# Performance work log

Hardware: AMD Instinct MI355X
Metric: run time of the kernel (lower is better)

## Reference

```python
import jax, jax.numpy as jnp
import numpy as np

NUM_HEADS = 16
HEAD_DIM = 64  # d_model // num_heads = 1024 // 16
NUM_BUCKETS = 20


def setup_inputs() -> dict:
    key = jax.random.key(0)
    ks = jax.random.split(key, 5)
    B, S, D = 2, 2048, 1024
    v = jax.random.normal(ks[0], (B, S, D), dtype=jnp.float32)
    k = jax.random.normal(ks[1], (B, S, D), dtype=jnp.float32)
    q = jax.random.normal(ks[2], (B, S, D), dtype=jnp.float32)
    mask = jax.random.randint(ks[3], (B, S, S), 0, 2).astype(jnp.bool_)
    diff_matrix = jax.random.randint(ks[4], (B, S, S), 0, NUM_BUCKETS)
    rel_bias = jax.random.normal(jax.random.fold_in(key, 7), (NUM_BUCKETS, NUM_HEADS), dtype=jnp.float32)
    return {"v": v, "k": k, "q": q, "mask": mask, "diff_matrix": diff_matrix, "rel_bias": rel_bias}


def _split_heads(x):
    B, S, _ = x.shape
    return x.reshape(B, S, NUM_HEADS, HEAD_DIM).transpose(0, 2, 1, 3)  # [B,H,S,hd]


def reference(v, k, q, mask, diff_matrix, rel_bias):
    B, S, D = q.shape
    qh, kh, vh = _split_heads(q), _split_heads(k), _split_heads(v)
    scale = 1.0 / jnp.sqrt(jnp.float32(HEAD_DIM))
    scores = jnp.einsum('bhqd,bhkd->bhqk', qh, kh) * scale  # [B,H,S,S]
    # relative bias: gather [B,S,S,H] -> [B,H,S,S]
    bias = rel_bias[diff_matrix].transpose(0, 3, 1, 2)
    att = jax.nn.silu(scores + bias)
    att = jnp.where(mask[:, None, :, :], att, 0.0)
    av = jnp.einsum('bhqk,bhkd->bhqd', att, vh)  # [B,H,S,hd]
    return av.transpose(0, 2, 1, 3).reshape(B, S, D)
```

## Files before the change

kernel.cpp:

```cpp
#include <hip/hip_runtime.h>
#include <hip/hip_fp16.h>
#include <cstdint>
#include <cstddef>

#define SEQ 2048
#define DM 1024
#define NH 16
#define NB 20

typedef _Float16 half8 __attribute__((ext_vector_type(8)));
typedef _Float16 half4 __attribute__((ext_vector_type(4)));
typedef _Float16 h2v __attribute__((ext_vector_type(2)));
typedef float f32x4 __attribute__((ext_vector_type(4)));
typedef int i32x4 __attribute__((ext_vector_type(4)));
typedef unsigned int u32;
typedef unsigned int u32x2 __attribute__((ext_vector_type(2)));

#define KF_HALVES 4194304
#define VF_HALVES 4194304

__global__ __launch_bounds__(256) void pa_prep(
    const float* __restrict__ v, const float* __restrict__ k,
    const int* __restrict__ diff, const int* __restrict__ mask,
    _Float16* __restrict__ KF, _Float16* __restrict__ VF,
    unsigned char* __restrict__ PB) {
  const int bid = blockIdx.x, tid = threadIdx.x;
  if (bid < 2048) {
    int img = bid >> 4;
    int bb = img >> 6, kt = img & 63;
    int tix = ((bid & 15) << 8) | tid;
    int r = tix >> 7;
    int c0 = (tix & 127) << 3;
    const float* src = k + ((size_t)(bb * SEQ + kt * 32 + r)) * DM + c0;
    f32x4 a = *(const f32x4*)src;
    f32x4 c = *(const f32x4*)(src + 4);
    half8 o = {(_Float16)a[0], (_Float16)a[1], (_Float16)a[2], (_Float16)a[3],
               (_Float16)c[0], (_Float16)c[1], (_Float16)c[2], (_Float16)c[3]};
    int h = c0 >> 6, dh = (c0 >> 5) & 1, g4 = (c0 >> 3) & 3;
    int k2 = r >> 4, l16 = r & 15;
    int lane = g4 * 16 + l16;
    size_t off = ((size_t)((bb * 16 + h) * 64 + kt)) * 2048 + (k2 * 2 + dh) * 512 + lane * 8;
    *(half8*)(KF + off) = o;
  } else if (bid < 3072) {
    int b3 = bid - 2048;
    int img = b3 >> 3;
    int bb = img >> 6, kt = img & 63;
    int tix = ((b3 & 7) << 8) | tid;
    int kq = tix >> 8;
    int k2 = kq >> 2, g4 = kq & 3;
    int d0 = (tix & 255) << 2;
    const float* src = v + ((size_t)(bb * SEQ + kt * 32 + k2 * 16 + g4 * 4)) * DM + d0;
    f32x4 m0 = *(const f32x4*)(src);
    f32x4 m1 = *(const f32x4*)(src + DM);
    f32x4 m2 = *(const f32x4*)(src + 2 * DM);
    f32x4 m3 = *(const f32x4*)(src + 3 * DM);
#pragma unroll
    for (int i = 0; i < 4; ++i) {
      int d = d0 + i;
      int l16 = d & 15, dt = (d >> 4) & 3, dtp = dt >> 1, w = dt & 1, h = d >> 6;
      int lane = g4 * 16 + l16;
      half4 o = {(_Float16)m0[i], (_Float16)m1[i], (_Float16)m2[i], (_Float16)m3[i]};
      size_t off = ((size_t)((bb * 16 + h) * 64 + kt)) * 2048 + (k2 * 2 + dtp) * 512 + lane * 8 + w * 4;
      *(half4*)(VF + off) = o;
    }
  } else {
    int b4 = bid - 3072;
    int job = b4 >> 5;
    int bb = job >> 6, qblk = job & 63;
    int tix = ((b4 & 31) << 8) | tid;
    int kt = tix >> 7;
    int rem = tix & 127;
    int g4 = rem & 3, l16 = (rem >> 2) & 15, qs = rem >> 6;
    int lane = g4 * 16 + l16;
    int qrow = qblk * 32 + qs * 16 + l16;
    size_t rowbase = ((size_t)(bb * SEQ + qrow)) * SEQ;
    u32x2 wds;
#pragma unroll
    for (int k2 = 0; k2 < 2; ++k2) {
      int kk = kt * 32 + k2 * 16 + g4 * 4;
      i32x4 dv = *(const i32x4*)(diff + rowbase + kk);
      i32x4 mv = *(const i32x4*)(mask + rowbase + kk);
      u32 wd = 0;
#pragma unroll
      for (int r = 0; r < 4; ++r) {
        u32 byte = mv[r] ? ((u32)dv[r] << 2) : 80u;
        wd |= byte << (8 * r);
      }
      wds[k2] = wd;
    }
    size_t off = ((size_t)job) * 65536 + (size_t)kt * 1024 + (size_t)lane * 16 + (size_t)qs * 8;
    *(u32x2*)(PB + off) = wds;
  }
}

__device__ __forceinline__ half4 silu4(const f32x4& s, u32 u, int rbi) {
  float b0 = __int_as_float(__builtin_amdgcn_ds_bpermute((int)(u & 0xffu), rbi));
  float b1 = __int_as_float(__builtin_amdgcn_ds_bpermute((int)((u >> 8) & 0xffu), rbi));
  float b2 = __int_as_float(__builtin_amdgcn_ds_bpermute((int)((u >> 16) & 0xffu), rbi));
  float b3 = __int_as_float(__builtin_amdgcn_ds_bpermute((int)(u >> 24), rbi));
  h2v x01 = __builtin_bit_cast(h2v, __builtin_amdgcn_cvt_pkrtz(s[0], s[1])) +
            __builtin_bit_cast(h2v, __builtin_amdgcn_cvt_pkrtz(b0, b1));
  h2v x23 = __builtin_bit_cast(h2v, __builtin_amdgcn_cvt_pkrtz(s[2], s[3])) +
            __builtin_bit_cast(h2v, __builtin_amdgcn_cvt_pkrtz(b2, b3));
  const h2v NL2E = {(_Float16)-1.44269504f, (_Float16)-1.44269504f};
  const h2v ONE = {(_Float16)1.0f, (_Float16)1.0f};
  h2v m01 = x01 * NL2E, m23 = x23 * NL2E;
  h2v e01 = __builtin_bit_cast(h2v, h2exp2(__builtin_bit_cast(__half2, m01)));
  h2v e23 = __builtin_bit_cast(h2v, h2exp2(__builtin_bit_cast(__half2, m23)));
  h2v d01 = e01 + ONE, d23 = e23 + ONE;
  h2v y01 = x01 * __builtin_bit_cast(h2v, h2rcp(__builtin_bit_cast(__half2, d01)));
  h2v y23 = x23 * __builtin_bit_cast(h2v, h2rcp(__builtin_bit_cast(__half2, d23)));
  return (half4){y01[0], y01[1], y23[0], y23[1]};
}

__global__ __launch_bounds__(256, 4) void pa_main(
    const _Float16* __restrict__ KF, const _Float16* __restrict__ VF,
    const unsigned char* __restrict__ PB, const float* __restrict__ q,
    const float* __restrict__ relbias, float* __restrict__ out) {
  const int tid = threadIdx.x, lane = tid & 63, wid = tid >> 6;
  const int l16 = lane & 15, g4 = lane >> 4;
  const int L = (blockIdx.x & 7) * 128 + (blockIdx.x >> 3);
  const int h = L & 15;
  const int qgrp = (L >> 4) & 15;
  const int ksp = (L >> 8) & 1;
  const int b = L >> 9;
  const int qblk = qgrp * 4 + wid;
  const int qbase = qblk * 32;

  const float rbv = (lane < NB) ? relbias[lane * NH + h] : -30000.0f;
  const int rbi = __float_as_int(rbv);

  half8 qf[2][2];
#pragma unroll
  for (int qs = 0; qs < 2; ++qs)
#pragma unroll
    for (int dh = 0; dh < 2; ++dh) {
      const float* s = q + ((size_t)(b * SEQ + qbase + qs * 16 + l16)) * DM + h * 64 + dh * 32 + g4 * 8;
      f32x4 a = *(const f32x4*)s;
      f32x4 c = *(const f32x4*)(s + 4);
      qf[qs][dh] = {(_Float16)(a[0] * 0.125f), (_Float16)(a[1] * 0.125f),
                    (_Float16)(a[2] * 0.125f), (_Float16)(a[3] * 0.125f),
                    (_Float16)(c[0] * 0.125f), (_Float16)(c[1] * 0.125f),
                    (_Float16)(c[2] * 0.125f), (_Float16)(c[3] * 0.125f)};
    }

  const f32x4 zf = {0.f, 0.f, 0.f, 0.f};
  f32x4 acc[2][4];
#pragma unroll
  for (int qs = 0; qs < 2; ++qs)
#pragma unroll
    for (int dt = 0; dt < 4; ++dt) acc[qs][dt] = zf;

  const _Float16* kfb = KF + ((size_t)((b * 16 + h) * 64 + ksp * 32)) * 2048 + lane * 8;
  const _Float16* vfb = VF + ((size_t)((b * 16 + h) * 64 + ksp * 32)) * 2048 + lane * 8;
  const unsigned char* pbb = PB + ((size_t)(b * 64 + qblk)) * 65536 + (size_t)(ksp * 32) * 1024 + lane * 16;

#pragma unroll 2
  for (int t = 0; t < 32; ++t) {
    half8 kfr[4], vvr[4];
#pragma unroll
    for (int j = 0; j < 4; ++j) {
      kfr[j] = *(const half8*)(kfb + (size_t)t * 2048 + j * 512);
      vvr[j] = *(const half8*)(vfb + (size_t)t * 2048 + j * 512);
    }
    i32x4 pq = *(const i32x4*)(pbb + (size_t)t * 1024);

#pragma unroll
    for (int k2 = 0; k2 < 2; ++k2) {
      f32x4 sa[2];
#pragma unroll
      for (int qs = 0; qs < 2; ++qs) {
        sa[qs] = __builtin_amdgcn_mfma_f32_16x16x32_f16(kfr[k2 * 2 + 0], qf[qs][0], zf, 0, 0, 0);
        sa[qs] = __builtin_amdgcn_mfma_f32_16x16x32_f16(kfr[k2 * 2 + 1], qf[qs][1], sa[qs], 0, 0, 0);
      }
      half4 pf[2];
      pf[0] = silu4(sa[0], (u32)pq[k2], rbi);
      pf[1] = silu4(sa[1], (u32)pq[2 + k2], rbi);

      half4 vf0 = __builtin_shufflevector(vvr[k2 * 2 + 0], vvr[k2 * 2 + 0], 0, 1, 2, 3);
      half4 vf1 = __builtin_shufflevector(vvr[k2 * 2 + 0], vvr[k2 * 2 + 0], 4, 5, 6, 7);
      half4 vf2 = __builtin_shufflevector(vvr[k2 * 2 + 1], vvr[k2 * 2 + 1], 0, 1, 2, 3);
      half4 vf3 = __builtin_shufflevector(vvr[k2 * 2 + 1], vvr[k2 * 2 + 1], 4, 5, 6, 7);
#pragma unroll
      for (int qs = 0; qs < 2; ++qs) {
        acc[qs][0] = __builtin_amdgcn_mfma_f32_16x16x16f16(pf[qs], vf0, acc[qs][0], 0, 0, 0);
        acc[qs][1] = __builtin_amdgcn_mfma_f32_16x16x16f16(pf[qs], vf1, acc[qs][1], 0, 0, 0);
        acc[qs][2] = __builtin_amdgcn_mfma_f32_16x16x16f16(pf[qs], vf2, acc[qs][2], 0, 0, 0);
        acc[qs][3] = __builtin_amdgcn_mfma_f32_16x16x16f16(pf[qs], vf3, acc[qs][3], 0, 0, 0);
      }
    }
  }

#pragma unroll
  for (int qs = 0; qs < 2; ++qs)
#pragma unroll
    for (int dt = 0; dt < 4; ++dt)
#pragma unroll
      for (int r = 0; r < 4; ++r) {
        int qrow = qbase + qs * 16 + g4 * 4 + r;
        int d = h * 64 + dt * 16 + l16;
        atomicAdd(&out[((size_t)(b * SEQ) + qrow) * DM + d], acc[qs][dt][r]);
      }
}

extern "C" void kernel_launch(void* const* d_in, const int* in_sizes, int n_in,
                              void* d_out, int out_size, void* d_ws, size_t ws_size,
                              hipStream_t stream) {
  const float* v = (const float*)d_in[0];
  const float* k = (const float*)d_in[1];
  const float* q = (const float*)d_in[2];
  const int* mask = (const int*)d_in[3];
  const int* diff = (const int*)d_in[4];
  const float* relbias = (const float*)d_in[5];
  float* out = (float*)d_out;

  _Float16* KF = (_Float16*)d_ws;
  _Float16* VF = KF + KF_HALVES;
  unsigned char* PB = (unsigned char*)(VF + VF_HALVES);
  if (ws_size < (size_t)25165824) return;

  (void)hipMemsetAsync(d_out, 0, (size_t)out_size * sizeof(float), stream);
  pa_prep<<<7168, 256, 0, stream>>>(v, k, diff, mask, KF, VF, PB);
  pa_main<<<1024, 256, 0, stream>>>(KF, VF, PB, q, relbias, out);
}
```

Measured before the change: 105.8 us.

## Double-buffer K/V/bias tile loads in registers and hoist bias permutes

Restructures the main loop into an explicit register double-buffer, issuing global loads for the next tile before computing the current one so memory latency overlaps the MFMA and SiLU work. The four bias-lookup permutes per quarter are hoisted to the start of each tile so they issue together ahead of the score MFMAs. Launch bounds drop from 4 to 3 waves-per-SIMD occupancy to give room for the extra registers. The last iteration redundantly reloads tile 31 to avoid a branch, and the lower occupancy may reduce latency hiding across waves.

```diff
diff --git a/kernel.cpp b/kernel.cpp
--- a/kernel.cpp
+++ b/kernel.cpp
@@ -93,15 +93,9 @@
   }
 }
 
-__device__ __forceinline__ half4 silu4(const f32x4& s, u32 u, int rbi) {
-  float b0 = __int_as_float(__builtin_amdgcn_ds_bpermute((int)(u & 0xffu), rbi));
-  float b1 = __int_as_float(__builtin_amdgcn_ds_bpermute((int)((u >> 8) & 0xffu), rbi));
-  float b2 = __int_as_float(__builtin_amdgcn_ds_bpermute((int)((u >> 16) & 0xffu), rbi));
-  float b3 = __int_as_float(__builtin_amdgcn_ds_bpermute((int)(u >> 24), rbi));
-  h2v x01 = __builtin_bit_cast(h2v, __builtin_amdgcn_cvt_pkrtz(s[0], s[1])) +
-            __builtin_bit_cast(h2v, __builtin_amdgcn_cvt_pkrtz(b0, b1));
-  h2v x23 = __builtin_bit_cast(h2v, __builtin_amdgcn_cvt_pkrtz(s[2], s[3])) +
-            __builtin_bit_cast(h2v, __builtin_amdgcn_cvt_pkrtz(b2, b3));
+__device__ __forceinline__ half4 silu4b(const f32x4& s, h2v b01, h2v b23) {
+  h2v x01 = __builtin_bit_cast(h2v, __builtin_amdgcn_cvt_pkrtz(s[0], s[1])) + b01;
+  h2v x23 = __builtin_bit_cast(h2v, __builtin_amdgcn_cvt_pkrtz(s[2], s[3])) + b23;
   const h2v NL2E = {(_Float16)-1.44269504f, (_Float16)-1.44269504f};
   const h2v ONE = {(_Float16)1.0f, (_Float16)1.0f};
   h2v m01 = x01 * NL2E, m23 = x23 * NL2E;
@@ -113,7 +107,50 @@
   return (half4){y01[0], y01[1], y23[0], y23[1]};
 }
 
-__global__ __launch_bounds__(256, 4) void pa_main(
+__device__ __forceinline__ void compute_tile(
+    const half8 (&kfr)[4], const half8 (&vvr)[4], const i32x4& pq,
+    const half8 (&qf)[2][2], f32x4 (&acc)[2][4], int rbi) {
+  const f32x4 zf = {0.f, 0.f, 0.f, 0.f};
+  h2v bias[2][2][2];
+#pragma unroll
+  for (int qs = 0; qs < 2; ++qs)
+#pragma unroll
+    for (int k2 = 0; k2 < 2; ++k2) {
+      u32 u = (u32)pq[qs * 2 + k2];
+      float b0 = __int_as_float(__builtin_amdgcn_ds_bpermute((int)(u & 0xffu), rbi));
+      float b1 = __int_as_float(__builtin_amdgcn_ds_bpermute((int)((u >> 8) & 0xffu), rbi));
+      float b2 = __int_as_float(__builtin_amdgcn_ds_bpermute((int)((u >> 16) & 0xffu), rbi));
+      float b3 = __int_as_float(__builtin_amdgcn_ds_bpermute((int)(u >> 24), rbi));
+      bias[qs][k2][0] = __builtin_bit_cast(h2v, __builtin_amdgcn_cvt_pkrtz(b0, b1));
+      bias[qs][k2][1] = __builtin_bit_cast(h2v, __builtin_amdgcn_cvt_pkrtz(b2, b3));
+    }
+#pragma unroll
+  for (int k2 = 0; k2 < 2; ++k2) {
+    f32x4 sa[2];
+#pragma unroll
+    for (int qs = 0; qs < 2; ++qs) {
+      sa[qs] = __builtin_amdgcn_mfma_f32_16x16x32_f16(kfr[k2 * 2 + 0], qf[qs][0], zf, 0, 0, 0);
+      sa[qs] = __builtin_amdgcn_mfma_f32_16x16x32_f16(kfr[k2 * 2 + 1], qf[qs][1], sa[qs], 0, 0, 0);
+    }
+    half4 pf[2];
+    pf[0] = silu4b(sa[0], bias[0][k2][0], bias[0][k2][1]);
+    pf[1] = silu4b(sa[1], bias[1][k2][0], bias[1][k2][1]);
+
+    half4 vf0 = __builtin_shufflevector(vvr[k2 * 2 + 0], vvr[k2 * 2 + 0], 0, 1, 2, 3);
+    half4 vf1 = __builtin_shufflevector(vvr[k2 * 2 + 0], vvr[k2 * 2 + 0], 4, 5, 6, 7);
+    half4 vf2 = __builtin_shufflevector(vvr[k2 * 2 + 1], vvr[k2 * 2 + 1], 0, 1, 2, 3);
+    half4 vf3 = __builtin_shufflevector(vvr[k2 * 2 + 1], vvr[k2 * 2 + 1], 4, 5, 6, 7);
+#pragma unroll
+    for (int qs = 0; qs < 2; ++qs) {
+      acc[qs][0] = __builtin_amdgcn_mfma_f32_16x16x16f16(pf[qs], vf0, acc[qs][0], 0, 0, 0);
+      acc[qs][1] = __builtin_amdgcn_mfma_f32_16x16x16f16(pf[qs], vf1, acc[qs][1], 0, 0, 0);
+      acc[qs][2] = __builtin_amdgcn_mfma_f32_16x16x16f16(pf[qs], vf2, acc[qs][2], 0, 0, 0);
+      acc[qs][3] = __builtin_amdgcn_mfma_f32_16x16x16f16(pf[qs], vf3, acc[qs][3], 0, 0, 0);
+    }
+  }
+}
+
+__global__ __launch_bounds__(256, 3) void pa_main(
     const _Float16* __restrict__ KF, const _Float16* __restrict__ VF,
     const unsigned char* __restrict__ PB, const float* __restrict__ q,
     const float* __restrict__ relbias, float* __restrict__ out) {
@@ -144,52 +181,36 @@
                     (_Float16)(c[2] * 0.125f), (_Float16)(c[3] * 0.125f)};
     }
 
-  const f32x4 zf = {0.f, 0.f, 0.f, 0.f};
   f32x4 acc[2][4];
 #pragma unroll
   for (int qs = 0; qs < 2; ++qs)
 #pragma unroll
-    for (int dt = 0; dt < 4; ++dt) acc[qs][dt] = zf;
+    for (int dt = 0; dt < 4; ++dt) acc[qs][dt] = (f32x4){0.f, 0.f, 0.f, 0.f};
 
   const _Float16* kfb = KF + ((size_t)((b * 16 + h) * 64 + ksp * 32)) * 2048 + lane * 8;
   const _Float16* vfb = VF + ((size_t)((b * 16 + h) * 64 + ksp * 32)) * 2048 + lane * 8;
   const unsigned char* pbb = PB + ((size_t)(b * 64 + qblk)) * 65536 + (size_t)(ksp * 32) * 1024 + lane * 16;
 
-#pragma unroll 2
-  for (int t = 0; t < 32; ++t) {
-    half8 kfr[4], vvr[4];
-#pragma unroll
-    for (int j = 0; j < 4; ++j) {
-      kfr[j] = *(const half8*)(kfb + (size_t)t * 2048 + j * 512);
-      vvr[j] = *(const half8*)(vfb + (size_t)t * 2048 + j * 512);
-    }
-    i32x4 pq = *(const i32x4*)(pbb + (size_t)t * 1024);
-
-#pragma unroll
-    for (int k2 = 0; k2 < 2; ++k2) {
-      f32x4 sa[2];
-#pragma unroll
-      for (int qs = 0; qs < 2; ++qs) {
-        sa[qs] = __builtin_amdgcn_mfma_f32_16x16x32_f16(kfr[k2 * 2 + 0], qf[qs][0], zf, 0, 0, 0);
-        sa[qs] = __builtin_amdgcn_mfma_f32_16x16x32_f16(kfr[k2 * 2 + 1], qf[qs][1], sa[qs], 0, 0, 0);
-      }
-      half4 pf[2];
-      pf[0] = silu4(sa[0], (u32)pq[k2], rbi);
-      pf[1] = silu4(sa[1], (u32)pq[2 + k2], rbi);
-
-      half4 vf0 = __builtin_shufflevector(vvr[k2 * 2 + 0], vvr[k2 * 2 + 0], 0, 1, 2, 3);
-      half4 vf1 = __builtin_shufflevector(vvr[k2 * 2 + 0], vvr[k2 * 2 + 0], 4, 5, 6, 7);
-      half4 vf2 = __builtin_shufflevector(vvr[k2 * 2 + 1], vvr[k2 * 2 + 1], 0, 1, 2, 3);
-      half4 vf3 = __builtin_shufflevector(vvr[k2 * 2 + 1], vvr[k2 * 2 + 1], 4, 5, 6, 7);
-#pragma unroll
-      for (int qs = 0; qs < 2; ++qs) {
-        acc[qs][0] = __builtin_amdgcn_mfma_f32_16x16x16f16(pf[qs], vf0, acc[qs][0], 0, 0, 0);
-        acc[qs][1] = __builtin_amdgcn_mfma_f32_16x16x16f16(pf[qs], vf1, acc[qs][1], 0, 0, 0);
-        acc[qs][2] = __builtin_amdgcn_mfma_f32_16x16x16f16(pf[qs], vf2, acc[qs][2], 0, 0, 0);
-        acc[qs][3] = __builtin_amdgcn_mfma_f32_16x16x16f16(pf[qs], vf3, acc[qs][3], 0, 0, 0);
-      }
-    }
+#define LOAD_TILE(T, KR, VR, PQ)                                       \
+  do {                                                                 \
+    _Pragma("unroll") for (int j = 0; j < 4; ++j) {                    \
+      KR[j] = *(const half8*)(kfb + (size_t)(T) * 2048 + j * 512);     \
+      VR[j] = *(const half8*)(vfb + (size_t)(T) * 2048 + j * 512);     \
+    }                                                                  \
+    PQ = *(const i32x4*)(pbb + (size_t)(T) * 1024);                    \
+  } while (0)
+
+  half8 kA[4], vA[4], kB[4], vB[4];
+  i32x4 pqA, pqB;
+  LOAD_TILE(0, kA, vA, pqA);
+  for (int t = 0; t < 32; t += 2) {
+    LOAD_TILE(t + 1, kB, vB, pqB);
+    compute_tile(kA, vA, pqA, qf, acc, rbi);
+    int tn = (t + 2 < 32) ? t + 2 : 31;
+    LOAD_TILE(tn, kA, vA, pqA);
+    compute_tile(kB, vB, pqB, qf, acc, rbi);
   }
+#undef LOAD_TILE
 
 #pragma unroll
   for (int qs = 0; qs < 2; ++qs)
```

Result: slower. 111.7 us (+5.6%).
